# Kernel tuning notes

Hardware: AMD Instinct MI355X
Metric: run time of the kernel (lower is better)

Reference implementation:

```python
import jax, jax.numpy as jnp
import numpy as np

H = 128; B = 128; NA = 32; N = B * NA; NH = 4; DH = H // NH; F = 2 * H + 3


def _ln(x, g, b, eps=1e-5):
    m = x.mean(-1, keepdims=True)
    v = ((x - m) ** 2).mean(-1, keepdims=True)
    return (x - m) / jnp.sqrt(v + eps) * g + b


def _silu(x):
    return x * jax.nn.sigmoid(x)


def setup_inputs() -> dict:
    key = jax.random.key(0)
    ks = jax.random.split(key, 16)
    def rn(i, shape, s=0.05):
        return jax.random.normal(ks[i], shape, jnp.float32) * s
    return dict(
        num_atoms=jnp.full((B,), NA, dtype=jnp.int32),
        elems=jax.random.randint(ks[0], (N,), 0, 119),
        cell=jnp.tile(10.0 * jnp.eye(3, dtype=jnp.float32), (B, 1)),  # [3B,3]
        coord=jax.random.uniform(ks[1], (N, 3), jnp.float32, 1.0, 9.0),
        emb=rn(2, (119, H), 1.0),
        ln_in_g=jnp.ones((H,), jnp.float32), ln_in_b=jnp.zeros((H,), jnp.float32),
        attn_in_w=rn(3, (H, 3 * H)), attn_in_b=jnp.zeros((3 * H,), jnp.float32),
        attn_out_w=rn(4, (H, H)), attn_out_b=jnp.zeros((H,), jnp.float32),
        ce_w1=rn(5, (3, H)), ce_b1=jnp.zeros((H,), jnp.float32),
        ce_w2=rn(6, (H, H)), ce_b2=jnp.zeros((H,), jnp.float32),
        ln_feat_g=jnp.ones((F,), jnp.float32), ln_feat_b=jnp.zeros((F,), jnp.float32),
        op_w1=rn(7, (F, H)), op_b1=jnp.zeros((H,), jnp.float32),
        op_ln1_g=jnp.ones((H,), jnp.float32), op_ln1_b=jnp.zeros((H,), jnp.float32),
        res_w1=rn(8, (H, H)), res_b1=jnp.zeros((H,), jnp.float32),
        res_ln_g=jnp.ones((H,), jnp.float32), res_ln_b=jnp.zeros((H,), jnp.float32),
        res_w2=rn(9, (H, H)), res_b2=jnp.zeros((H,), jnp.float32),
        op_ln2_g=jnp.ones((H,), jnp.float32), op_ln2_b=jnp.zeros((H,), jnp.float32),
        op_w3=rn(10, (H, 3)), op_b3=jnp.zeros((3,), jnp.float32),
    )


def reference(num_atoms, elems, cell, coord, emb, ln_in_g, ln_in_b,
              attn_in_w, attn_in_b, attn_out_w, attn_out_b,
              ce_w1, ce_b1, ce_w2, ce_b2, ln_feat_g, ln_feat_b,
              op_w1, op_b1, op_ln1_g, op_ln1_b,
              res_w1, res_b1, res_ln_g, res_ln_b, res_w2, res_b2,
              op_ln2_g, op_ln2_b, op_w3, op_b3):
    n = coord.shape[0]
    # atom embedding + input LayerNorm
    x = _ln(emb[elems], ln_in_g, ln_in_b)
    # unbatched multihead self-attention over all atoms (seq_len = n)
    qkv = x @ attn_in_w + attn_in_b
    q, k, v = jnp.split(qkv, 3, axis=-1)
    q = q.reshape(n, NH, DH); k = k.reshape(n, NH, DH); v = v.reshape(n, NH, DH)
    a = jax.nn.softmax(jnp.einsum('qhd,khd->hqk', q, k) / np.float32(np.sqrt(DH)), axis=-1)
    x = jnp.einsum('hqk,khd->qhd', a, v).reshape(n, H) @ attn_out_w + attn_out_b
    # cell encoder on [3B,3] rows
    cf = _silu(cell @ ce_w1 + ce_b1) @ ce_w2 + ce_b2
    bidx = jnp.repeat(jnp.arange(num_atoms.shape[0]), num_atoms, total_repeat_length=n)
    # torch: cf.repeat(B,1)[batch_idx] == cf[batch_idx] since batch_idx < B
    comb = _ln(jnp.concatenate([x, cf[bidx], coord], axis=-1), ln_feat_g, ln_feat_b)
    # offset predictor
    h = _silu(_ln(comb @ op_w1 + op_b1, op_ln1_g, op_ln1_b))
    h = h + (_silu(_ln(h @ res_w1 + res_b1, res_ln_g, res_ln_b)) @ res_w2 + res_b2)
    h = _ln(h, op_ln2_g, op_ln2_b)
    offset = jnp.tanh(h @ op_w3 + op_b3) * 0.01
    perturbed = coord + offset
    # per-molecule clamp: segment gather of per-cell-row min/max replaces the python loop
    c3 = cell.reshape(-1, 3, 3)           # [B,3,3]
    cmin = c3.min(axis=2) + 1e-6          # [B,3]
    cmax = c3.max(axis=2) - 1e-6          # [B,3]
    return jnp.clip(perturbed, cmin[bidx], cmax[bidx])
```

## Files before the change

kernel.cpp:

```cpp
#include <hip/hip_runtime.h>
#include <hip/hip_bf16.h>
#include <math.h>
#include <stdint.h>

#define NATOMS 4096
#define HD     128
#define NHEAD  4
#define DHEAD  32
#define FDIM   259
#define BATCH  128
#define H3X    384
#define SPLIT  4

typedef __attribute__((ext_vector_type(8))) short short8;
typedef __attribute__((ext_vector_type(4))) float float4v;
typedef __attribute__((ext_vector_type(16))) float f32x16;

__device__ __forceinline__ ushort f2bf(float f) {
    uint32_t u = __float_as_uint(f);
    return (ushort)((u + 0x7fffu + ((u >> 16) & 1u)) >> 16);
}
__device__ __forceinline__ float b2f(ushort u) {
    return __uint_as_float(((uint32_t)u) << 16);
}
__device__ __forceinline__ f32x16 z16() {
    f32x16 v;
#pragma unroll
    for (int i = 0; i < 16; i++) v[i] = 0.f;
    return v;
}

#define NB_PACK 528
#define NB_CELL 128
__global__ __launch_bounds__(256) void k_setup(
        const int* __restrict__ num_atoms, const float* __restrict__ cell,
        const float* __restrict__ qkvw, const float* __restrict__ aow,
        const float* __restrict__ op1w, const float* __restrict__ r1w,
        const float* __restrict__ r2w,
        const float* __restrict__ ce_w1, const float* __restrict__ ce_b1,
        const float* __restrict__ ce_w2, const float* __restrict__ ce_b2,
        int* __restrict__ bidx, float* __restrict__ cmin, float* __restrict__ cmax,
        ushort* __restrict__ Wqkv, ushort* __restrict__ Wao,
        ushort* __restrict__ Wop1, ushort* __restrict__ Wr1, ushort* __restrict__ Wr2,
        float* __restrict__ CF) {
    __shared__ float hs[HD];
    __shared__ int start[BATCH + 1];
    const int t = threadIdx.x;
    if (blockIdx.x < NB_PACK) {
        int idx = blockIdx.x * 256 + t;
        if (idx < 49152) {
            int k = idx / 384, n = idx - k * 384;
            Wqkv[n * 128 + k] = f2bf(qkvw[idx]);
        } else if (idx < 65536) {
            int j = idx - 49152; int k = j >> 7, n = j & 127;
            Wao[n * 128 + k] = f2bf(aow[j]);
        } else if (idx < 98688) {
            int j = idx - 65536; int k = j >> 7, n = j & 127;
            Wop1[n * 288 + k] = f2bf(op1w[j]);
        } else if (idx < 102400) {
            int j = idx - 98688; int n = j & 127, k = 259 + (j >> 7);
            Wop1[n * 288 + k] = 0;
        } else if (idx < 118784) {
            int j = idx - 102400; int k = j >> 7, n = j & 127;
            Wr1[n * 128 + k] = f2bf(r1w[j]);
        } else {
            int j = idx - 118784; int k = j >> 7, n = j & 127;
            Wr2[n * 128 + k] = f2bf(r2w[j]);
        }
    } else if (blockIdx.x < NB_PACK + NB_CELL) {
        int r = blockIdx.x - NB_PACK;
        if (t < 128) {
            float c0 = cell[r * 3 + 0], c1 = cell[r * 3 + 1], c2 = cell[r * 3 + 2];
            float h = c0 * ce_w1[t] + c1 * ce_w1[HD + t] + c2 * ce_w1[2 * HD + t] + ce_b1[t];
            h = h / (1.f + __expf(-h));
            hs[t] = h;
        }
        __syncthreads();
        if (t < 128) {
            float acc = ce_b2[t];
#pragma unroll 8
            for (int k = 0; k < HD; k++) acc += hs[k] * ce_w2[k * HD + t];
            CF[r * HD + t] = acc;
        }
    } else {
        if (t == 0) {
            int pos = 0;
            for (int b = 0; b < BATCH; b++) { start[b] = pos; pos += num_atoms[b]; }
            start[BATCH] = pos;
        }
        __syncthreads();
        if (t < 128) {
            int s = min(start[t], NATOMS), e = min(start[t + 1], NATOMS);
            for (int j = s; j < e; j++) bidx[j] = t;
            if (t == 0) {
                int total = min(start[BATCH], NATOMS);
                for (int j = total; j < NATOMS; j++) bidx[j] = BATCH - 1;
            }
        }
        for (int rr = t; rr < BATCH * 3; rr += 256) {
            float a0 = cell[rr * 3 + 0], a1 = cell[rr * 3 + 1], a2 = cell[rr * 3 + 2];
            cmin[rr] = fminf(a0, fminf(a1, a2)) + 1e-6f;
            cmax[rr] = fmaxf(a0, fmaxf(a1, a2)) - 1e-6f;
        }
    }
}

__global__ __launch_bounds__(256) void k_qkv(const int* __restrict__ elems,
                                             const float* __restrict__ emb,
                                             const float* __restrict__ lg,
                                             const float* __restrict__ lb,
                                             const ushort* __restrict__ Wt,
                                             const float* __restrict__ bias,
                                             ushort* __restrict__ Qb, ushort* __restrict__ Kb,
                                             ushort* __restrict__ VTb2) {
    __shared__ alignas(16) ushort Af[4][64][8];
    __shared__ alignas(16) ushort vt[128][16];
    const int t = threadIdx.x, w = t >> 6, lane = t & 63, quad = lane >> 4, lq = lane & 15;
    const int rb = blockIdx.x * 16;
    {
        int row = t >> 4, seg = t & 15;
        int e = elems[rb + row];
        const float* ep = emb + (size_t)e * HD + seg * 8;
        float v[8]; float s = 0.f, ss = 0.f;
#pragma unroll
        for (int j = 0; j < 8; j++) { v[j] = ep[j]; s += v[j]; ss += v[j] * v[j]; }
#pragma unroll
        for (int m = 1; m < 16; m <<= 1) { s += __shfl_xor(s, m); ss += __shfl_xor(ss, m); }
        float mean = s * (1.f / HD);
        float inv = rsqrtf(ss * (1.f / HD) - mean * mean + 1e-5f);
        ushort o[8];
#pragma unroll
        for (int j = 0; j < 8; j++)
            o[j] = f2bf((v[j] - mean) * inv * lg[seg * 8 + j] + lb[seg * 8 + j]);
        *(uint4*)&Af[seg >> 2][(seg & 3) * 16 + row][0] = *(uint4*)o;
    }
    __syncthreads();
    float4v acc[6];
#pragma unroll
    for (int i = 0; i < 6; i++) acc[i] = (float4v){0.f, 0.f, 0.f, 0.f};
#pragma unroll
    for (int kt = 0; kt < 4; kt++) {
        short8 af = *(const short8*)&Af[kt][lane][0];
#pragma unroll
        for (int i = 0; i < 6; i++) {
            int nt = w * 6 + i;
            short8 wf = *(const short8*)(Wt + (size_t)(lq + 16 * nt) * HD + kt * 32 + quad * 8);
            acc[i] = __builtin_amdgcn_mfma_f32_16x16x32_bf16(af, wf, acc[i], 0, 0, 0);
        }
    }
#pragma unroll
    for (int i = 0; i < 6; i++) {
        int col = lq + 16 * (w * 6 + i);
        float bb = bias[col];
#pragma unroll
        for (int r = 0; r < 4; r++) {
            float c = acc[i][r] + bb;
            int rowin = quad * 4 + r;
            int row = rb + rowin;
            if (col < 128) {
                Qb[(size_t)(((col >> 5) * NATOMS) + row) * 32 + (col & 31)] = f2bf(c * 0.25503483f);
            } else if (col < 256) {
                int cc = col - 128;
                Kb[(size_t)(((cc >> 5) * NATOMS) + row) * 32 + (cc & 31)] = f2bf(c);
            } else {
                vt[col - 256][rowin] = f2bf(c);
            }
        }
    }
    __syncthreads();
    if (t < 128) {
        int hh = t >> 5, d = t & 31;
        uint4 a0 = *(const uint4*)&vt[t][0];
        uint4 a1 = *(const uint4*)&vt[t][8];
        ushort* dst = VTb2 + ((size_t)(hh * 64 + (rb >> 6)) * 32 + d) * 64 + (rb & 63);
        *(uint4*)(dst) = a0;
        *(uint4*)(dst + 8) = a1;
    }
}

__global__ __launch_bounds__(256) void k_attn(const ushort* __restrict__ Qb,
                                              const ushort* __restrict__ Kb,
                                              const ushort* __restrict__ VTb2,
                                              ushort* __restrict__ Opart,
                                              float* __restrict__ lpart) {
    __shared__ alignas(16) ushort P_s[4][32 * 72];
    __shared__ alignas(16) float OL[2][32 * 36];
    __shared__ float LL[2][32];
    const int t = threadIdx.x, w = t >> 6, lane = t & 63;
    const int l31 = lane & 31, hi = lane >> 5;
    const int qt = w & 1, kh2 = w >> 1;
    const int h = blockIdx.y, sp = blockIdx.z;
    const int q0 = blockIdx.x * 64;
    const int qrow = q0 + qt * 32 + l31;

    short8 qf0 = *(const short8*)(Qb + (size_t)(h * NATOMS + qrow) * 32 + hi * 8);
    short8 qf1 = *(const short8*)(Qb + (size_t)(h * NATOMS + qrow) * 32 + 16 + hi * 8);
    f32x16 O = z16();
    float lp = 0.f;
    ushort* Pw = &P_s[w][0];
    const int kstart = sp * (NATOMS / SPLIT) + kh2 * 64;

    for (int ck = 0; ck < (NATOMS / SPLIT) / 128; ck++) {
        int kb = kstart + ck * 128;
        const ushort* vbase = VTb2 + ((size_t)(h * 64 + (kb >> 6)) * 32 + l31) * 64;
#pragma unroll
        for (int kt = 0; kt < 2; kt++) {
            int kk = kb + kt * 32;
            const ushort* kp = Kb + (size_t)(h * NATOMS + kk + l31) * 32 + hi * 8;
            short8 kf0 = *(const short8*)(kp);
            short8 kf1 = *(const short8*)(kp + 16);
            f32x16 S = z16();
            S = __builtin_amdgcn_mfma_f32_32x32x16_bf16(kf0, qf0, S, 0, 0, 0);
            S = __builtin_amdgcn_mfma_f32_32x32x16_bf16(kf1, qf1, S, 0, 0, 0);
#pragma unroll
            for (int c = 0; c < 4; c++) {
                float p0 = exp2f(S[4 * c + 0]);
                float p1 = exp2f(S[4 * c + 1]);
                float p2 = exp2f(S[4 * c + 2]);
                float p3 = exp2f(S[4 * c + 3]);
                lp += (p0 + p1) + (p2 + p3);
                uint32_t u0 = __float_as_uint(p0) + 0x8000u;
                uint32_t u1 = __float_as_uint(p1) + 0x8000u;
                uint32_t u2 = __float_as_uint(p2) + 0x8000u;
                uint32_t u3 = __float_as_uint(p3) + 0x8000u;
                uint2 u;
                u.x = __builtin_amdgcn_perm(u1, u0, 0x07060302u);
                u.y = __builtin_amdgcn_perm(u3, u2, 0x07060302u);
                *(uint2*)(&Pw[l31 * 72 + kt * 32 + c * 8 + hi * 4]) = u;
            }
#pragma unroll
            for (int wd = 0; wd < 2; wd++) {
                int koff = kt * 32 + wd * 16;
                short8 vf = *(const short8*)(vbase + koff + hi * 8);
                short8 pf = *(const short8*)(&Pw[l31 * 72 + koff + hi * 8]);
                O = __builtin_amdgcn_mfma_f32_32x32x16_bf16(vf, pf, O, 0, 0, 0);
            }
        }
    }
    lp += __shfl_xor(lp, 32);
    if (kh2 == 0) {
#pragma unroll
        for (int c = 0; c < 4; c++) {
            float4 f = {O[4 * c + 0], O[4 * c + 1], O[4 * c + 2], O[4 * c + 3]};
            *(float4*)(&OL[qt][l31 * 36 + c * 8 + hi * 4]) = f;
        }
        if (hi == 0) LL[qt][l31] = lp;
    }
    __syncthreads();
    if (kh2 == 1) {
        lp += LL[qt][l31];
#pragma unroll
        for (int c = 0; c < 4; c++) {
            float4 f = *(const float4*)(&OL[qt][l31 * 36 + c * 8 + hi * 4]);
            float o0 = O[4 * c + 0] + f.x, o1 = O[4 * c + 1] + f.y;
            float o2 = O[4 * c + 2] + f.z, o3 = O[4 * c + 3] + f.w;
            uint2 u;
            u.x = (uint32_t)f2bf(o0) | ((uint32_t)f2bf(o1) << 16);
            u.y = (uint32_t)f2bf(o2) | ((uint32_t)f2bf(o3) << 16);
            *(uint2*)(Opart + (size_t)(sp * NATOMS + qrow) * HD + h * 32 + c * 8 + hi * 4) = u;
        }
        if (hi == 0) lpart[sp * (NHEAD * NATOMS) + h * NATOMS + qrow] = lp;
    }
}

__global__ __launch_bounds__(512) void k_back(
        const ushort* __restrict__ Opart, const float* __restrict__ lpart,
        const ushort* __restrict__ Wao, const float* __restrict__ aob,
        const float* __restrict__ CF, const float* __restrict__ coord,
        const int* __restrict__ bidx,
        const float* __restrict__ fg, const float* __restrict__ fb,
        const ushort* __restrict__ Wop1, const float* __restrict__ op1b,
        const float* __restrict__ l1g, const float* __restrict__ l1b,
        const ushort* __restrict__ Wr1, const float* __restrict__ r1b,
        const float* __restrict__ rlg, const float* __restrict__ rlb,
        const ushort* __restrict__ Wr2, const float* __restrict__ r2b,
        const float* __restrict__ l2g, const float* __restrict__ l2b,
        const float* __restrict__ w3, const float* __restrict__ b3,
        const float* __restrict__ cmin, const float* __restrict__ cmax,
        float* __restrict__ out) {
    __shared__ alignas(16) ushort AF1[9][64][8];
    __shared__ alignas(16) ushort AF2[4][64][8];
    __shared__ alignas(16) ushort AF3[4][64][8];
    __shared__ float RED[8][16][4];
    __shared__ float REDC[16][2];
    __shared__ float COORDS[16][3];
    const int t = threadIdx.x, w = t >> 6, lane = t & 63, quad = lane >> 4, lq = lane & 15;
    const int rb = blockIdx.x * 16;
    const int col = lq + 16 * w;

    const int arow = rb + lq;
    float4v a0 = {0.f, 0.f, 0.f, 0.f};
#pragma unroll
    for (int h = 0; h < 4; h++) {
        float l = 0.f;
#pragma unroll
        for (int s = 0; s < SPLIT; s++) l += lpart[s * (NHEAD * NATOMS) + h * NATOMS + arow];
        float inv = 1.f / l;
        float pv[8];
#pragma unroll
        for (int j = 0; j < 8; j++) pv[j] = 0.f;
#pragma unroll
        for (int s = 0; s < SPLIT; s++) {
            short8 ov = *(const short8*)(Opart + (size_t)(s * NATOMS + arow) * HD + h * 32 + quad * 8);
#pragma unroll
            for (int j = 0; j < 8; j++) pv[j] += b2f((ushort)ov[j]);
        }
        short8 af;
#pragma unroll
        for (int j = 0; j < 8; j++) af[j] = (short)f2bf(pv[j] * inv);
        short8 w0 = *(const short8*)(Wao + (size_t)col * HD + h * 32 + quad * 8);
        a0 = __builtin_amdgcn_mfma_f32_16x16x32_bf16(af, w0, a0, 0, 0, 0);
    }
    float x1[4];
#pragma unroll
    for (int r = 0; r < 4; r++) x1[r] = a0[r] + aob[col];

    float cfv[4];
#pragma unroll
    for (int r = 0; r < 4; r++) cfv[r] = CF[bidx[rb + quad * 4 + r] * HD + col];
#pragma unroll
    for (int r = 0; r < 4; r++) {
        float s1 = x1[r] + cfv[r];
        float s2 = x1[r] * x1[r] + cfv[r] * cfv[r];
#pragma unroll
        for (int m = 1; m < 16; m <<= 1) { s1 += __shfl_xor(s1, m); s2 += __shfl_xor(s2, m); }
        if (lq == 0) { RED[w][quad * 4 + r][0] = s1; RED[w][quad * 4 + r][1] = s2; }
    }
    if (t < 16) {
        float c0 = coord[(rb + t) * 3 + 0], c1 = coord[(rb + t) * 3 + 1], c2 = coord[(rb + t) * 3 + 2];
        COORDS[t][0] = c0; COORDS[t][1] = c1; COORDS[t][2] = c2;
        REDC[t][0] = c0 + c1 + c2; REDC[t][1] = c0 * c0 + c1 * c1 + c2 * c2;
    }
    if (t < 64) { uint4 z = {0, 0, 0, 0}; *(uint4*)&AF1[8][t][0] = z; }
    __syncthreads();
#pragma unroll
    for (int r = 0; r < 4; r++) {
        int ri = quad * 4 + r;
        float s1 = REDC[ri][0], s2 = REDC[ri][1];
#pragma unroll
        for (int ww = 0; ww < 8; ww++) { s1 += RED[ww][ri][0]; s2 += RED[ww][ri][1]; }
        float mn = s1 * (1.f / FDIM);
        float iv = rsqrtf(s2 * (1.f / FDIM) - mn * mn + 1e-5f);
        float vx = (x1[r] - mn) * iv * fg[col] + fb[col];
        float vc = (cfv[r] - mn) * iv * fg[col + 128] + fb[col + 128];
        AF1[col >> 5][((col >> 3) & 3) * 16 + ri][col & 7] = f2bf(vx);
        int c2 = col + 128;
        AF1[c2 >> 5][((c2 >> 3) & 3) * 16 + ri][c2 & 7] = f2bf(vc);
    }
    if (t < 16) {
        float s1 = REDC[t][0], s2 = REDC[t][1];
#pragma unroll
        for (int ww = 0; ww < 8; ww++) { s1 += RED[ww][t][0]; s2 += RED[ww][t][1]; }
        float mn = s1 * (1.f / FDIM);
        float iv = rsqrtf(s2 * (1.f / FDIM) - mn * mn + 1e-5f);
#pragma unroll
        for (int c = 0; c < 3; c++)
            AF1[8][t][c] = f2bf((COORDS[t][c] - mn) * iv * fg[256 + c] + fb[256 + c]);
    }
    __syncthreads();

    float4v cv = {0.f, 0.f, 0.f, 0.f};
#pragma unroll
    for (int kt = 0; kt < 9; kt++) {
        short8 af = *(const short8*)&AF1[kt][lane][0];
        short8 w0 = *(const short8*)(Wop1 + (size_t)col * 288 + kt * 32 + quad * 8);
        cv = __builtin_amdgcn_mfma_f32_16x16x32_bf16(af, w0, cv, 0, 0, 0);
    }
    float h0[4];
#pragma unroll
    for (int r = 0; r < 4; r++) {
        h0[r] = cv[r] + op1b[col];
        float s1 = h0[r], s2 = h0[r] * h0[r];
#pragma unroll
        for (int m = 1; m < 16; m <<= 1) { s1 += __shfl_xor(s1, m); s2 += __shfl_xor(s2, m); }
        if (lq == 0) { RED[w][quad * 4 + r][0] = s1; RED[w][quad * 4 + r][1] = s2; }
    }
    __syncthreads();
#pragma unroll
    for (int r = 0; r < 4; r++) {
        int ri = quad * 4 + r;
        float s1 = 0.f, s2 = 0.f;
#pragma unroll
        for (int ww = 0; ww < 8; ww++) { s1 += RED[ww][ri][0]; s2 += RED[ww][ri][1]; }
        float mn = s1 * (1.f / HD);
        float iv = rsqrtf(s2 * (1.f / HD) - mn * mn + 1e-5f);
        float o = (h0[r] - mn) * iv * l1g[col] + l1b[col];
        o = o / (1.f + __expf(-o));
        AF2[col >> 5][((col >> 3) & 3) * 16 + ri][col & 7] = f2bf(o);
    }
    __syncthreads();

    float4v dv = {0.f, 0.f, 0.f, 0.f};
#pragma unroll
    for (int kt = 0; kt < 4; kt++) {
        short8 af = *(const short8*)&AF2[kt][lane][0];
        short8 w0 = *(const short8*)(Wr1 + (size_t)col * HD + kt * 32 + quad * 8);
        dv = __builtin_amdgcn_mfma_f32_16x16x32_bf16(af, w0, dv, 0, 0, 0);
    }
    float e0[4];
#pragma unroll
    for (int r = 0; r < 4; r++) {
        e0[r] = dv[r] + r1b[col];
        float s1 = e0[r], s2 = e0[r] * e0[r];
#pragma unroll
        for (int m = 1; m < 16; m <<= 1) { s1 += __shfl_xor(s1, m); s2 += __shfl_xor(s2, m); }
        if (lq == 0) { RED[w][quad * 4 + r][0] = s1; RED[w][quad * 4 + r][1] = s2; }
    }
    __syncthreads();
#pragma unroll
    for (int r = 0; r < 4; r++) {
        int ri = quad * 4 + r;
        float s1 = 0.f, s2 = 0.f;
#pragma unroll
        for (int ww = 0; ww < 8; ww++) { s1 += RED[ww][ri][0]; s2 += RED[ww][ri][1]; }
        float mn = s1 * (1.f / HD);
        float iv = rsqrtf(s2 * (1.f / HD) - mn * mn + 1e-5f);
        float o = (e0[r] - mn) * iv * rlg[col] + rlb[col];
        o = o / (1.f + __expf(-o));
        AF3[col >> 5][((col >> 3) & 3) * 16 + ri][col & 7] = f2bf(o);
    }
    __syncthreads();

    float4v fv = {0.f, 0.f, 0.f, 0.f};
#pragma unroll
    for (int kt = 0; kt < 4; kt++) {
        short8 af = *(const short8*)&AF3[kt][lane][0];
        short8 w0 = *(const short8*)(Wr2 + (size_t)col * HD + kt * 32 + quad * 8);
        fv = __builtin_amdgcn_mfma_f32_16x16x32_bf16(af, w0, fv, 0, 0, 0);
    }
    float g0r[4];
#pragma unroll
    for (int r = 0; r < 4; r++) {
        int ri = quad * 4 + r;
        float rs = b2f(AF2[col >> 5][((col >> 3) & 3) * 16 + ri][col & 7]);
        g0r[r] = fv[r] + r2b[col] + rs;
        float s1 = g0r[r], s2 = g0r[r] * g0r[r];
#pragma unroll
        for (int m = 1; m < 16; m <<= 1) { s1 += __shfl_xor(s1, m); s2 += __shfl_xor(s2, m); }
        if (lq == 0) { RED[w][ri][0] = s1; RED[w][ri][1] = s2; }
    }
    __syncthreads();
    float tp[4][3];
#pragma unroll
    for (int r = 0; r < 4; r++) {
        int ri = quad * 4 + r;
        float s1 = 0.f, s2 = 0.f;
#pragma unroll
        for (int ww = 0; ww < 8; ww++) { s1 += RED[ww][ri][0]; s2 += RED[ww][ri][1]; }
        float mn = s1 * (1.f / HD);
        float iv = rsqrtf(s2 * (1.f / HD) - mn * mn + 1e-5f);
        float h2 = (g0r[r] - mn) * iv * l2g[col] + l2b[col];
#pragma unroll
        for (int c = 0; c < 3; c++) {
            float v = h2 * w3[col * 3 + c];
#pragma unroll
            for (int m = 1; m < 16; m <<= 1) v += __shfl_xor(v, m);
            tp[r][c] = v;
        }
    }
    __syncthreads();
    if (lq == 0) {
#pragma unroll
        for (int r = 0; r < 4; r++) {
            RED[w][quad * 4 + r][0] = tp[r][0];
            RED[w][quad * 4 + r][1] = tp[r][1];
            RED[w][quad * 4 + r][2] = tp[r][2];
        }
    }
    __syncthreads();
    if (t < 16) {
        int bi = bidx[rb + t];
#pragma unroll
        for (int c = 0; c < 3; c++) {
            float sv = 0.f;
#pragma unroll
            for (int ww = 0; ww < 8; ww++) sv += RED[ww][t][c];
            float off = tanhf(sv + b3[c]) * 0.01f;
            float pert = COORDS[t][c] + off;
            pert = fminf(fmaxf(pert, cmin[bi * 3 + c]), cmax[bi * 3 + c]);
            out[(rb + t) * 3 + c] = pert;
        }
    }
}

extern "C" void kernel_launch(void* const* d_in, const int* in_sizes, int n_in,
                              void* d_out, int out_size, void* d_ws, size_t ws_size,
                              hipStream_t stream) {
    const int* num_atoms = (const int*)d_in[0];
    const int* elems = (const int*)d_in[1];
    const float* cell = (const float*)d_in[2];
    const float* coord = (const float*)d_in[3];
    const float* emb = (const float*)d_in[4];
    const float* ln_in_g = (const float*)d_in[5];
    const float* ln_in_b = (const float*)d_in[6];
    const float* attn_in_w = (const float*)d_in[7];
    const float* attn_in_b = (const float*)d_in[8];
    const float* attn_out_w = (const float*)d_in[9];
    const float* attn_out_b = (const float*)d_in[10];
    const float* ce_w1 = (const float*)d_in[11];
    const float* ce_b1 = (const float*)d_in[12];
    const float* ce_w2 = (const float*)d_in[13];
    const float* ce_b2 = (const float*)d_in[14];
    const float* ln_feat_g = (const float*)d_in[15];
    const float* ln_feat_b = (const float*)d_in[16];
    const float* op_w1 = (const float*)d_in[17];
    const float* op_b1 = (const float*)d_in[18];
    const float* op_ln1_g = (const float*)d_in[19];
    const float* op_ln1_b = (const float*)d_in[20];
    const float* res_w1 = (const float*)d_in[21];
    const float* res_b1 = (const float*)d_in[22];
    const float* res_ln_g = (const float*)d_in[23];
    const float* res_ln_b = (const float*)d_in[24];
    const float* res_w2 = (const float*)d_in[25];
    const float* res_b2 = (const float*)d_in[26];
    const float* op_ln2_g = (const float*)d_in[27];
    const float* op_ln2_b = (const float*)d_in[28];
    const float* op_w3 = (const float*)d_in[29];
    const float* op_b3 = (const float*)d_in[30];

    char* ws = (char*)d_ws;
    const size_t MB = 1u << 20;
    ushort* Qb = (ushort*)(ws);
    ushort* Kb = (ushort*)(ws + 1 * MB);
    ushort* VTb2 = (ushort*)(ws + 2 * MB);
    ushort* Opart = (ushort*)(ws + 3 * MB);
    float* lpart = (float*)(ws + 7 * MB);
    int* bidx = (int*)(ws + 7 * MB + (256u << 10));
    float* cmin = (float*)(ws + 7 * MB + (272u << 10));
    float* cmax = (float*)(ws + 7 * MB + (274u << 10));
    float* CF = (float*)(ws + 7 * MB + (276u << 10));
    ushort* Wqkv = (ushort*)(ws + 7 * MB + (340u << 10));
    ushort* Wao = (ushort*)(ws + 7 * MB + (436u << 10));
    ushort* Wop1 = (ushort*)(ws + 7 * MB + (468u << 10));
    ushort* Wr1 = (ushort*)(ws + 7 * MB + (540u << 10));
    ushort* Wr2 = (ushort*)(ws + 7 * MB + (572u << 10));

    k_setup<<<NB_PACK + NB_CELL + 1, 256, 0, stream>>>(
        num_atoms, cell, attn_in_w, attn_out_w, op_w1, res_w1, res_w2,
        ce_w1, ce_b1, ce_w2, ce_b2,
        bidx, cmin, cmax, Wqkv, Wao, Wop1, Wr1, Wr2, CF);
    k_qkv<<<256, 256, 0, stream>>>(elems, emb, ln_in_g, ln_in_b, Wqkv, attn_in_b,
                                   Qb, Kb, VTb2);
    k_attn<<<dim3(NATOMS / 64, NHEAD, SPLIT), 256, 0, stream>>>(Qb, Kb, VTb2, Opart, lpart);
    k_back<<<256, 512, 0, stream>>>(Opart, lpart, Wao, attn_out_b, CF, coord, bidx,
                                    ln_feat_g, ln_feat_b, Wop1, op_b1, op_ln1_g, op_ln1_b,
                                    Wr1, res_b1, res_ln_g, res_ln_b, Wr2, res_b2,
                                    op_ln2_g, op_ln2_b, op_w3, op_b3, cmin, cmax,
                                    (float*)d_out);
}
```

Baseline: 180.2 us.

## Move non-QKV setup work into attention grid and split QKV blocks

The setup kernel now only packs the QKV weights. Packing of the other weights, the cell encoder, bidx and the clamp bounds move into an extra z-slice of the attention grid, so they run alongside attention instead of on the critical path before QKV. The QKV kernel gets twice as many blocks, each computing half of the output columns, for more parallelism. The softmax probability packing uses the hardware v_cvt_pk_bf16_f32 instruction instead of manual rounding and permutes. In exchange, the extra blocks share the attention launch, and the bf16 conversion may round differently from the old manual path.

Measured after the change: 175.4 us. -2.7%, faster.

```diff
diff --git a/kernel.cpp b/kernel.cpp
--- a/kernel.cpp
+++ b/kernel.cpp
@@ -30,79 +30,11 @@
     return v;
 }
 
-#define NB_PACK 528
-#define NB_CELL 128
-__global__ __launch_bounds__(256) void k_setup(
-        const int* __restrict__ num_atoms, const float* __restrict__ cell,
-        const float* __restrict__ qkvw, const float* __restrict__ aow,
-        const float* __restrict__ op1w, const float* __restrict__ r1w,
-        const float* __restrict__ r2w,
-        const float* __restrict__ ce_w1, const float* __restrict__ ce_b1,
-        const float* __restrict__ ce_w2, const float* __restrict__ ce_b2,
-        int* __restrict__ bidx, float* __restrict__ cmin, float* __restrict__ cmax,
-        ushort* __restrict__ Wqkv, ushort* __restrict__ Wao,
-        ushort* __restrict__ Wop1, ushort* __restrict__ Wr1, ushort* __restrict__ Wr2,
-        float* __restrict__ CF) {
-    __shared__ float hs[HD];
-    __shared__ int start[BATCH + 1];
-    const int t = threadIdx.x;
-    if (blockIdx.x < NB_PACK) {
-        int idx = blockIdx.x * 256 + t;
-        if (idx < 49152) {
-            int k = idx / 384, n = idx - k * 384;
-            Wqkv[n * 128 + k] = f2bf(qkvw[idx]);
-        } else if (idx < 65536) {
-            int j = idx - 49152; int k = j >> 7, n = j & 127;
-            Wao[n * 128 + k] = f2bf(aow[j]);
-        } else if (idx < 98688) {
-            int j = idx - 65536; int k = j >> 7, n = j & 127;
-            Wop1[n * 288 + k] = f2bf(op1w[j]);
-        } else if (idx < 102400) {
-            int j = idx - 98688; int n = j & 127, k = 259 + (j >> 7);
-            Wop1[n * 288 + k] = 0;
-        } else if (idx < 118784) {
-            int j = idx - 102400; int k = j >> 7, n = j & 127;
-            Wr1[n * 128 + k] = f2bf(r1w[j]);
-        } else {
-            int j = idx - 118784; int k = j >> 7, n = j & 127;
-            Wr2[n * 128 + k] = f2bf(r2w[j]);
-        }
-    } else if (blockIdx.x < NB_PACK + NB_CELL) {
-        int r = blockIdx.x - NB_PACK;
-        if (t < 128) {
-            float c0 = cell[r * 3 + 0], c1 = cell[r * 3 + 1], c2 = cell[r * 3 + 2];
-            float h = c0 * ce_w1[t] + c1 * ce_w1[HD + t] + c2 * ce_w1[2 * HD + t] + ce_b1[t];
-            h = h / (1.f + __expf(-h));
-            hs[t] = h;
-        }
-        __syncthreads();
-        if (t < 128) {
-            float acc = ce_b2[t];
-#pragma unroll 8
-            for (int k = 0; k < HD; k++) acc += hs[k] * ce_w2[k * HD + t];
-            CF[r * HD + t] = acc;
-        }
-    } else {
-        if (t == 0) {
-            int pos = 0;
-            for (int b = 0; b < BATCH; b++) { start[b] = pos; pos += num_atoms[b]; }
-            start[BATCH] = pos;
-        }
-        __syncthreads();
-        if (t < 128) {
-            int s = min(start[t], NATOMS), e = min(start[t + 1], NATOMS);
-            for (int j = s; j < e; j++) bidx[j] = t;
-            if (t == 0) {
-                int total = min(start[BATCH], NATOMS);
-                for (int j = total; j < NATOMS; j++) bidx[j] = BATCH - 1;
-            }
-        }
-        for (int rr = t; rr < BATCH * 3; rr += 256) {
-            float a0 = cell[rr * 3 + 0], a1 = cell[rr * 3 + 1], a2 = cell[rr * 3 + 2];
-            cmin[rr] = fminf(a0, fminf(a1, a2)) + 1e-6f;
-            cmax[rr] = fmaxf(a0, fmaxf(a1, a2)) - 1e-6f;
-        }
-    }
+__global__ __launch_bounds__(256) void k_setup(const float* __restrict__ qkvw,
+                                               ushort* __restrict__ Wqkv) {
+    int idx = blockIdx.x * 256 + threadIdx.x;
+    int k = idx / 384, n = idx - k * 384;
+    Wqkv[n * 128 + k] = f2bf(qkvw[idx]);
 }
 
 __global__ __launch_bounds__(256) void k_qkv(const int* __restrict__ elems,
@@ -116,7 +48,8 @@
     __shared__ alignas(16) ushort Af[4][64][8];
     __shared__ alignas(16) ushort vt[128][16];
     const int t = threadIdx.x, w = t >> 6, lane = t & 63, quad = lane >> 4, lq = lane & 15;
-    const int rb = blockIdx.x * 16;
+    const int rg = blockIdx.x >> 1, half = blockIdx.x & 1;
+    const int rb = rg * 16;
     {
         int row = t >> 4, seg = t & 15;
         int e = elems[rb + row];
@@ -135,22 +68,22 @@
         *(uint4*)&Af[seg >> 2][(seg & 3) * 16 + row][0] = *(uint4*)o;
     }
     __syncthreads();
-    float4v acc[6];
-#pragma unroll
-    for (int i = 0; i < 6; i++) acc[i] = (float4v){0.f, 0.f, 0.f, 0.f};
+    float4v acc[3];
+#pragma unroll
+    for (int i = 0; i < 3; i++) acc[i] = (float4v){0.f, 0.f, 0.f, 0.f};
 #pragma unroll
     for (int kt = 0; kt < 4; kt++) {
         short8 af = *(const short8*)&Af[kt][lane][0];
 #pragma unroll
-        for (int i = 0; i < 6; i++) {
-            int nt = w * 6 + i;
+        for (int i = 0; i < 3; i++) {
+            int nt = half * 12 + w * 3 + i;
             short8 wf = *(const short8*)(Wt + (size_t)(lq + 16 * nt) * HD + kt * 32 + quad * 8);
             acc[i] = __builtin_amdgcn_mfma_f32_16x16x32_bf16(af, wf, acc[i], 0, 0, 0);
         }
     }
 #pragma unroll
-    for (int i = 0; i < 6; i++) {
-        int col = lq + 16 * (w * 6 + i);
+    for (int i = 0; i < 3; i++) {
+        int col = lq + 16 * (half * 12 + w * 3 + i);
         float bb = bias[col];
 #pragma unroll
         for (int r = 0; r < 4; r++) {
@@ -168,7 +101,7 @@
         }
     }
     __syncthreads();
-    if (t < 128) {
+    if (half == 1 && t < 128) {
         int hh = t >> 5, d = t & 31;
         uint4 a0 = *(const uint4*)&vt[t][0];
         uint4 a1 = *(const uint4*)&vt[t][8];
@@ -182,11 +115,91 @@
                                               const ushort* __restrict__ Kb,
                                               const ushort* __restrict__ VTb2,
                                               ushort* __restrict__ Opart,
-                                              float* __restrict__ lpart) {
+                                              float* __restrict__ lpart,
+                                              const int* __restrict__ num_atoms,
+                                              const float* __restrict__ cell,
+                                              const float* __restrict__ aow,
+                                              const float* __restrict__ op1w,
+                                              const float* __restrict__ r1w,
+                                              const float* __restrict__ r2w,
+                                              const float* __restrict__ ce_w1,
+                                              const float* __restrict__ ce_b1,
+                                              const float* __restrict__ ce_w2,
+                                              const float* __restrict__ ce_b2,
+                                              int* __restrict__ bidx,
+                                              float* __restrict__ cmin,
+                                              float* __restrict__ cmax,
+                                              ushort* __restrict__ Wao,
+                                              ushort* __restrict__ Wop1,
+                                              ushort* __restrict__ Wr1,
+                                              ushort* __restrict__ Wr2,
+                                              float* __restrict__ CF) {
     __shared__ alignas(16) ushort P_s[4][32 * 72];
     __shared__ alignas(16) float OL[2][32 * 36];
     __shared__ float LL[2][32];
-    const int t = threadIdx.x, w = t >> 6, lane = t & 63;
+    const int t = threadIdx.x;
+
+    if (blockIdx.z == SPLIT) {
+        float* hs = (float*)&P_s[0][0];
+        int* start = (int*)&P_s[1][0];
+        const int mid = blockIdx.y * 64 + blockIdx.x;
+        for (int j = mid * 256 + t; j < 86016; j += 65536) {
+            if (j < 16384) {
+                int k = j >> 7, n = j & 127;
+                Wao[n * 128 + k] = f2bf(aow[j]);
+            } else if (j < 49536) {
+                int jj = j - 16384; int k = jj >> 7, n = jj & 127;
+                Wop1[n * 288 + k] = f2bf(op1w[jj]);
+            } else if (j < 53248) {
+                int jj = j - 49536; int n = jj & 127, k = 259 + (jj >> 7);
+                Wop1[n * 288 + k] = 0;
+            } else if (j < 69632) {
+                int jj = j - 53248; int k = jj >> 7, n = jj & 127;
+                Wr1[n * 128 + k] = f2bf(r1w[jj]);
+            } else {
+                int jj = j - 69632; int k = jj >> 7, n = jj & 127;
+                Wr2[n * 128 + k] = f2bf(r2w[jj]);
+            }
+        }
+        if (mid < 128) {
+            if (t < 128) {
+                float c0 = cell[mid * 3 + 0], c1 = cell[mid * 3 + 1], c2 = cell[mid * 3 + 2];
+                float h = c0 * ce_w1[t] + c1 * ce_w1[HD + t] + c2 * ce_w1[2 * HD + t] + ce_b1[t];
+                h = h / (1.f + __expf(-h));
+                hs[t] = h;
+            }
+            __syncthreads();
+            if (t < 128) {
+                float acc = ce_b2[t];
+#pragma unroll 8
+                for (int k = 0; k < HD; k++) acc += hs[k] * ce_w2[k * HD + t];
+                CF[mid * HD + t] = acc;
+            }
+        } else if (mid == 128) {
+            if (t == 0) {
+                int pos = 0;
+                for (int b = 0; b < BATCH; b++) { start[b] = pos; pos += num_atoms[b]; }
+                start[BATCH] = pos;
+            }
+            __syncthreads();
+            if (t < 128) {
+                int s = min(start[t], NATOMS), e = min(start[t + 1], NATOMS);
+                for (int j = s; j < e; j++) bidx[j] = t;
+                if (t == 0) {
+                    int total = min(start[BATCH], NATOMS);
+                    for (int j = total; j < NATOMS; j++) bidx[j] = BATCH - 1;
+                }
+            }
+            for (int rr = t; rr < BATCH * 3; rr += 256) {
+                float a0 = cell[rr * 3 + 0], a1 = cell[rr * 3 + 1], a2 = cell[rr * 3 + 2];
+                cmin[rr] = fminf(a0, fminf(a1, a2)) + 1e-6f;
+                cmax[rr] = fmaxf(a0, fmaxf(a1, a2)) - 1e-6f;
+            }
+        }
+        return;
+    }
+
+    const int w = t >> 6, lane = t & 63;
     const int l31 = lane & 31, hi = lane >> 5;
     const int qt = w & 1, kh2 = w >> 1;
     const int h = blockIdx.y, sp = blockIdx.z;
@@ -219,13 +232,9 @@
                 float p2 = exp2f(S[4 * c + 2]);
                 float p3 = exp2f(S[4 * c + 3]);
                 lp += (p0 + p1) + (p2 + p3);
-                uint32_t u0 = __float_as_uint(p0) + 0x8000u;
-                uint32_t u1 = __float_as_uint(p1) + 0x8000u;
-                uint32_t u2 = __float_as_uint(p2) + 0x8000u;
-                uint32_t u3 = __float_as_uint(p3) + 0x8000u;
                 uint2 u;
-                u.x = __builtin_amdgcn_perm(u1, u0, 0x07060302u);
-                u.y = __builtin_amdgcn_perm(u3, u2, 0x07060302u);
+                asm("v_cvt_pk_bf16_f32 %0, %1, %2" : "=v"(u.x) : "v"(p0), "v"(p1));
+                asm("v_cvt_pk_bf16_f32 %0, %1, %2" : "=v"(u.y) : "v"(p2), "v"(p3));
                 *(uint2*)(&Pw[l31 * 72 + kt * 32 + c * 8 + hi * 4]) = u;
             }
 #pragma unroll
@@ -535,13 +544,14 @@
     ushort* Wr1 = (ushort*)(ws + 7 * MB + (540u << 10));
     ushort* Wr2 = (ushort*)(ws + 7 * MB + (572u << 10));
 
-    k_setup<<<NB_PACK + NB_CELL + 1, 256, 0, stream>>>(
-        num_atoms, cell, attn_in_w, attn_out_w, op_w1, res_w1, res_w2,
-        ce_w1, ce_b1, ce_w2, ce_b2,
-        bidx, cmin, cmax, Wqkv, Wao, Wop1, Wr1, Wr2, CF);
-    k_qkv<<<256, 256, 0, stream>>>(elems, emb, ln_in_g, ln_in_b, Wqkv, attn_in_b,
+    k_setup<<<192, 256, 0, stream>>>(attn_in_w, Wqkv);
+    k_qkv<<<512, 256, 0, stream>>>(elems, emb, ln_in_g, ln_in_b, Wqkv, attn_in_b,
                                    Qb, Kb, VTb2);
-    k_attn<<<dim3(NATOMS / 64, NHEAD, SPLIT), 256, 0, stream>>>(Qb, Kb, VTb2, Opart, lpart);
+    k_attn<<<dim3(NATOMS / 64, NHEAD, SPLIT + 1), 256, 0, stream>>>(
+        Qb, Kb, VTb2, Opart, lpart,
+        num_atoms, cell, attn_out_w, op_w1, res_w1, res_w2,
+        ce_w1, ce_b1, ce_w2, ce_b2, bidx, cmin, cmax,
+        Wao, Wop1, Wr1, Wr2, CF);
     k_back<<<256, 512, 0, stream>>>(Opart, lpart, Wao, attn_out_b, CF, coord, bidx,
                                     ln_feat_g, ln_feat_b, Wop1, op_b1, op_ln1_g, op_ln1_b,
                                     Wr1, res_b1, res_ln_g, res_ln_b, Wr2, res_b2,
```
